# Optimization experiments

Hardware: AMD Instinct MI355X
Metric: run time of the kernel (lower is better)

The kernel has to match this reference:

```python
import jax, jax.numpy as jnp
import numpy as np

GAMMA = 0.99
ETA = 0.1
PHI = 0.9
EPS_FLOOR_NEWTON = 1e-8
EPS_FLOOR_BETA = 1e-6
N_NEWTON = 20


def _epsilon_cosh(r):
    # r: [B, N] nonnegative residuals; per-row Newton solve for epsilon s.t.
    # mean(sinh(r/eps)) == 1 along axis 1.
    N = r.shape[1]
    r_max = jnp.maximum(jnp.max(r, axis=1, keepdims=True), EPS_FLOOR_NEWTON)
    eps = r_max / (jnp.log(jnp.asarray(2.0 * N, dtype=r.dtype)) + EPS_FLOOR_NEWTON)
    for _ in range(N_NEWTON):
        eps_safe = jnp.maximum(eps, EPS_FLOOR_NEWTON)
        u = r / eps_safe  # [B, N]
        val = jnp.mean(jnp.sinh(u), axis=1, keepdims=True) - 1.0
        grad = jnp.mean(jnp.cosh(u) * (-u / eps_safe), axis=1, keepdims=True)
        eps = eps - val / (grad - EPS_FLOOR_NEWTON)
    return jnp.maximum(eps, EPS_FLOOR_NEWTON)


def _update_spatial_weights(r_i, Lambda, it):
    # 'cosh' weighting potential branch of update_spatial_weights
    del it  # unused by the cosh branch
    eps_q = _epsilon_cosh(r_i)                       # [B, 1]
    beta = 1.0 / (eps_q + EPS_FLOOR_BETA)            # [B, 1]
    q = jnp.sinh(beta * r_i)                         # [B, N]
    q_max = jnp.max(q, axis=1, keepdims=True)
    q_norm = q / (q_max + 1e-20)
    lambda_it = PHI * q_norm + (1.0 - PHI)
    return GAMMA * Lambda + ETA * lambda_it


def setup_inputs() -> dict:
    key = jax.random.key(0)
    k1, k2, k3 = jax.random.split(key, 3)
    B, N = 2048, 8192
    y_pred = jax.random.normal(k1, (B, N), dtype=jnp.float32)
    y_true = jax.random.normal(k2, (B, N), dtype=jnp.float32)
    Lambda = jax.random.uniform(k3, (B, N), dtype=jnp.float32)
    return {"y_pred": y_pred, "y_true": y_true, "Lambda": Lambda, "it": 100}


def reference(y_pred, y_true, Lambda, it):
    r_i = jnp.abs(y_true - y_pred)
    # weights are computed on detached residuals
    updated_Lambda = _update_spatial_weights(jax.lax.stop_gradient(r_i), Lambda, it)
    loss = jnp.mean(jnp.square(updated_Lambda * r_i))
    return (loss, updated_Lambda)
```

## Files before the change

### kernel.cpp

```cpp
#include <hip/hip_runtime.h>
#include <math.h>

#define N_COLS 8192
#define BLOCK  256
#define NW     4
#define F4PT   (N_COLS / BLOCK / 4)
#define NBINS  1024
#define BPL    (NBINS / 64)

__global__ void zero_out_kernel(float* out) {
    if (threadIdx.x == 0 && blockIdx.x == 0) out[0] = 0.0f;
}

__global__ __launch_bounds__(BLOCK) void custom_loss_kernel(
        const float* __restrict__ y_pred,
        const float* __restrict__ y_true,
        const float* __restrict__ Lambda,
        float* __restrict__ out,
        float inv_total) {
    __shared__ unsigned int s_hist[NBINS];
    __shared__ float s_wmax[NW];
    __shared__ float s_part[NW];
    __shared__ float s_bcast[2];

    const int row  = blockIdx.x;
    const int tid  = threadIdx.x;
    const int lane = tid & 63;
    const int wid  = tid >> 6;
    const size_t base = (size_t)row * N_COLS;
    const float4* yp4 = (const float4*)(y_pred + base);
    const float4* yt4 = (const float4*)(y_true + base);

    float4 r[F4PT];
    float rmax = 0.0f;
    #pragma unroll
    for (int j = 0; j < F4PT; ++j) {
        const int g = j * BLOCK + tid;
        float4 a = yt4[g];
        float4 b = yp4[g];
        float4 rv;
        rv.x = fabsf(a.x - b.x); rv.y = fabsf(a.y - b.y);
        rv.z = fabsf(a.z - b.z); rv.w = fabsf(a.w - b.w);
        r[j] = rv;
        rmax = fmaxf(rmax, fmaxf(fmaxf(rv.x, rv.y), fmaxf(rv.z, rv.w)));
    }
    #pragma unroll
    for (int m = 32; m >= 1; m >>= 1) rmax = fmaxf(rmax, __shfl_xor(rmax, m, 64));
    #pragma unroll
    for (int i = 0; i < NBINS / BLOCK; ++i) s_hist[tid + i * BLOCK] = 0u;
    __syncthreads();
    if (lane == 0) s_wmax[wid] = rmax;
    __syncthreads();
    rmax = fmaxf(fmaxf(s_wmax[0], s_wmax[1]), fmaxf(s_wmax[2], s_wmax[3]));
    rmax = fmaxf(rmax, 1e-8f);

    const float hscale = (float)NBINS / rmax;
    #pragma unroll
    for (int j = 0; j < F4PT; ++j) {
        unsigned bx = min((unsigned)(r[j].x * hscale), (unsigned)(NBINS - 1));
        unsigned by = min((unsigned)(r[j].y * hscale), (unsigned)(NBINS - 1));
        unsigned bz = min((unsigned)(r[j].z * hscale), (unsigned)(NBINS - 1));
        unsigned bw = min((unsigned)(r[j].w * hscale), (unsigned)(NBINS - 1));
        atomicAdd(&s_hist[bx], 1u);
        atomicAdd(&s_hist[by], 1u);
        atomicAdd(&s_hist[bz], 1u);
        atomicAdd(&s_hist[bw], 1u);
    }
    __syncthreads();

    if (wid == 0) {
        float eps = rmax / (logf(2.0f * (float)N_COLS) + 1e-8f);
        const float binw = rmax * (1.0f / (float)NBINS);
        const float sc2  = 0.5f / (float)N_COLS;
        for (int it = 0; it < 20; ++it) {
            const float inv_eps = 1.0f / fmaxf(eps, 1e-8f);
            float fs = 0.0f, gs = 0.0f;
            #pragma unroll
            for (int k = 0; k < BPL; ++k) {
                const int b = lane + 64 * k;
                float n = (float)s_hist[b];
                float m = ((float)b + 0.5f) * binw;
                float u = m * inv_eps;
                float e  = __expf(u);
                float ei = __expf(-u);
                fs = fmaf(n, e - ei, fs);
                gs = fmaf(n * (e + ei), u, gs);
            }
            #pragma unroll
            for (int m2 = 32; m2 >= 1; m2 >>= 1) {
                fs += __shfl_xor(fs, m2, 64);
                gs += __shfl_xor(gs, m2, 64);
            }
            float val  = fmaf(fs, sc2, -1.0f);
            float grad = -(gs * sc2) * inv_eps;
            float delta = val / (grad - 1e-8f);
            eps -= delta;
            if (fabsf(delta) <= 1e-5f * eps) break;
        }
        eps = fmaxf(eps, 1e-8f);
        const float beta = 1.0f / (eps + 1e-6f);
        const float um = beta * rmax;
        const float qmax = 0.5f * (__expf(um) - __expf(-um));
        if (lane == 0) {
            s_bcast[0] = beta;
            s_bcast[1] = 1.0f / (qmax + 1e-20f);
        }
    }
    __syncthreads();
    const float beta     = s_bcast[0];
    const float inv_qmax = s_bcast[1];

    const float4* lam4 = (const float4*)(Lambda + base);
    float* outw = out + 1 + base;
    float s_loss = 0.0f;
    #pragma unroll
    for (int j = 0; j < F4PT; ++j) {
        const int g = j * BLOCK + tid;
        float4 L = lam4[g];
        float rr[4] = {r[j].x, r[j].y, r[j].z, r[j].w};
        float LL[4] = {L.x, L.y, L.z, L.w};
        #pragma unroll
        for (int c = 0; c < 4; ++c) {
            float u  = beta * rr[c];
            float q  = 0.5f * (__expf(u) - __expf(-u));
            float lam_it = fmaf(0.9f, q * inv_qmax, 0.1f);
            float uL = fmaf(0.99f, LL[c], 0.1f * lam_it);
            outw[(size_t)g * 4 + c] = uL;
            float t = uL * rr[c];
            s_loss = fmaf(t, t, s_loss);
        }
    }
    #pragma unroll
    for (int m = 32; m >= 1; m >>= 1) s_loss += __shfl_xor(s_loss, m, 64);
    __syncthreads();
    if (lane == 0) s_part[wid] = s_loss;
    __syncthreads();
    if (tid == 0) {
        float tot = (s_part[0] + s_part[1]) + (s_part[2] + s_part[3]);
        atomicAdd(out, tot * inv_total);
    }
}

extern "C" void kernel_launch(void* const* d_in, const int* in_sizes, int n_in,
                              void* d_out, int out_size, void* d_ws, size_t ws_size,
                              hipStream_t stream) {
    const float* y_pred = (const float*)d_in[0];
    const float* y_true = (const float*)d_in[1];
    const float* Lambda = (const float*)d_in[2];
    float* out = (float*)d_out;

    const int total = in_sizes[0];
    const int B = total / N_COLS;
    const float inv_total = 1.0f / (float)total;

    hipLaunchKernelGGL(zero_out_kernel, dim3(1), dim3(64), 0, stream, out);
    hipLaunchKernelGGL(custom_loss_kernel, dim3(B), dim3(BLOCK), 0, stream,
                       y_pred, y_true, Lambda, out, inv_total);
}
```

Measured before the change: 226.0 us.

## Bin residuals by float exponent bits and run Newton solve redundantly per wave

Histogram bins now come straight from the float bit pattern (a log-spaced range with a fixed offset), so binning no longer waits for the block-wide max reduction and can overlap it. Every wave now runs the Newton iteration itself on register-cached bins, which removes the serial single-wave phase and the broadcast barrier. Lambda is prefetched together with the residual loads. The cost is more registers (Lambda held in registers, bins per lane) and a fixed bin range that may clip very small or very large residuals, which can change accuracy.

```diff
diff --git a/kernel.cpp b/kernel.cpp
--- a/kernel.cpp
+++ b/kernel.cpp
@@ -1,12 +1,13 @@
 #include <hip/hip_runtime.h>
 #include <math.h>
 
-#define N_COLS 8192
-#define BLOCK  256
-#define NW     4
-#define F4PT   (N_COLS / BLOCK / 4)
-#define NBINS  1024
-#define BPL    (NBINS / 64)
+#define N_COLS  8192
+#define BLOCK   256
+#define VPT     (N_COLS / BLOCK)
+#define F4PT    (VPT / 4)
+#define NBINS   1024
+#define BIN_OFF 7360
+#define BPL     (NBINS / 64)
 
 __global__ void zero_out_kernel(float* out) {
     if (threadIdx.x == 0 && blockIdx.x == 0) out[0] = 0.0f;
@@ -18,26 +19,31 @@
         const float* __restrict__ Lambda,
         float* __restrict__ out,
         float inv_total) {
-    __shared__ unsigned int s_hist[NBINS];
-    __shared__ float s_wmax[NW];
-    __shared__ float s_part[NW];
-    __shared__ float s_bcast[2];
+    __shared__ unsigned s_hist[NBINS];
+    __shared__ float s_wmax[4];
+    __shared__ float s_part[4];
 
     const int row  = blockIdx.x;
     const int tid  = threadIdx.x;
     const int lane = tid & 63;
     const int wid  = tid >> 6;
     const size_t base = (size_t)row * N_COLS;
-    const float4* yp4 = (const float4*)(y_pred + base);
-    const float4* yt4 = (const float4*)(y_true + base);
+    const float4* yp4  = (const float4*)(y_pred + base);
+    const float4* yt4  = (const float4*)(y_true + base);
+    const float4* lam4 = (const float4*)(Lambda + base);
+
+    #pragma unroll
+    for (int i = 0; i < NBINS / BLOCK; ++i) s_hist[tid + i * BLOCK] = 0u;
+    __syncthreads();
 
     float4 r[F4PT];
+    float4 L[F4PT];
     float rmax = 0.0f;
     #pragma unroll
     for (int j = 0; j < F4PT; ++j) {
         const int g = j * BLOCK + tid;
-        float4 a = yt4[g];
-        float4 b = yp4[g];
+        float4 a = yt4[g], b = yp4[g];
+        L[j] = lam4[g];
         float4 rv;
         rv.x = fabsf(a.x - b.x); rv.y = fabsf(a.y - b.y);
         rv.z = fabsf(a.z - b.z); rv.w = fabsf(a.w - b.w);
@@ -45,80 +51,65 @@
         rmax = fmaxf(rmax, fmaxf(fmaxf(rv.x, rv.y), fmaxf(rv.z, rv.w)));
     }
     #pragma unroll
+    for (int j = 0; j < F4PT; ++j) {
+        float rv[4] = {r[j].x, r[j].y, r[j].z, r[j].w};
+        #pragma unroll
+        for (int c = 0; c < 4; ++c) {
+            int idx = (int)(__float_as_uint(rv[c]) >> 17) - BIN_OFF;
+            idx = min(max(idx, 0), NBINS - 1);
+            atomicAdd(&s_hist[idx], 1u);
+        }
+    }
+    #pragma unroll
     for (int m = 32; m >= 1; m >>= 1) rmax = fmaxf(rmax, __shfl_xor(rmax, m, 64));
-    #pragma unroll
-    for (int i = 0; i < NBINS / BLOCK; ++i) s_hist[tid + i * BLOCK] = 0u;
-    __syncthreads();
     if (lane == 0) s_wmax[wid] = rmax;
     __syncthreads();
-    rmax = fmaxf(fmaxf(s_wmax[0], s_wmax[1]), fmaxf(s_wmax[2], s_wmax[3]));
-    rmax = fmaxf(rmax, 1e-8f);
+    rmax = fmaxf(fmaxf(fmaxf(s_wmax[0], s_wmax[1]),
+                       fmaxf(s_wmax[2], s_wmax[3])), 1e-8f);
 
-    const float hscale = (float)NBINS / rmax;
+    float n[BPL], m[BPL];
     #pragma unroll
-    for (int j = 0; j < F4PT; ++j) {
-        unsigned bx = min((unsigned)(r[j].x * hscale), (unsigned)(NBINS - 1));
-        unsigned by = min((unsigned)(r[j].y * hscale), (unsigned)(NBINS - 1));
-        unsigned bz = min((unsigned)(r[j].z * hscale), (unsigned)(NBINS - 1));
-        unsigned bw = min((unsigned)(r[j].w * hscale), (unsigned)(NBINS - 1));
-        atomicAdd(&s_hist[bx], 1u);
-        atomicAdd(&s_hist[by], 1u);
-        atomicAdd(&s_hist[bz], 1u);
-        atomicAdd(&s_hist[bw], 1u);
+    for (int i = 0; i < BPL; ++i) {
+        const int b = lane + 64 * i;
+        n[i] = (float)s_hist[b];
+        m[i] = __uint_as_float(((unsigned)(b + BIN_OFF) << 17) | 0x10000u);
     }
-    __syncthreads();
+    float eps = rmax / (logf(2.0f * (float)N_COLS) + 1e-8f);
+    const float sc2 = 0.5f / (float)N_COLS;
+    for (int it = 0; it < 20; ++it) {
+        const float inv_eps = 1.0f / fmaxf(eps, 1e-8f);
+        float fs = 0.0f, gs = 0.0f;
+        #pragma unroll
+        for (int i = 0; i < BPL; ++i) {
+            float u  = m[i] * inv_eps;
+            float e  = __expf(u);
+            float ei = __expf(-u);
+            fs = fmaf(n[i], e - ei, fs);
+            gs = fmaf(n[i] * (e + ei), u, gs);
+        }
+        #pragma unroll
+        for (int s = 32; s >= 1; s >>= 1) {
+            fs += __shfl_xor(fs, s, 64);
+            gs += __shfl_xor(gs, s, 64);
+        }
+        float val  = fmaf(fs, sc2, -1.0f);
+        float grad = -(gs * sc2) * inv_eps;
+        float delta = val / (grad - 1e-8f);
+        eps -= delta;
+        if (fabsf(delta) <= 1e-5f * eps) break;
+    }
+    eps = fmaxf(eps, 1e-8f);
+    const float beta = 1.0f / (eps + 1e-6f);
+    const float um = beta * rmax;
+    const float inv_qmax = 1.0f / (0.5f * (__expf(um) - __expf(-um)) + 1e-20f);
 
-    if (wid == 0) {
-        float eps = rmax / (logf(2.0f * (float)N_COLS) + 1e-8f);
-        const float binw = rmax * (1.0f / (float)NBINS);
-        const float sc2  = 0.5f / (float)N_COLS;
-        for (int it = 0; it < 20; ++it) {
-            const float inv_eps = 1.0f / fmaxf(eps, 1e-8f);
-            float fs = 0.0f, gs = 0.0f;
-            #pragma unroll
-            for (int k = 0; k < BPL; ++k) {
-                const int b = lane + 64 * k;
-                float n = (float)s_hist[b];
-                float m = ((float)b + 0.5f) * binw;
-                float u = m * inv_eps;
-                float e  = __expf(u);
-                float ei = __expf(-u);
-                fs = fmaf(n, e - ei, fs);
-                gs = fmaf(n * (e + ei), u, gs);
-            }
-            #pragma unroll
-            for (int m2 = 32; m2 >= 1; m2 >>= 1) {
-                fs += __shfl_xor(fs, m2, 64);
-                gs += __shfl_xor(gs, m2, 64);
-            }
-            float val  = fmaf(fs, sc2, -1.0f);
-            float grad = -(gs * sc2) * inv_eps;
-            float delta = val / (grad - 1e-8f);
-            eps -= delta;
-            if (fabsf(delta) <= 1e-5f * eps) break;
-        }
-        eps = fmaxf(eps, 1e-8f);
-        const float beta = 1.0f / (eps + 1e-6f);
-        const float um = beta * rmax;
-        const float qmax = 0.5f * (__expf(um) - __expf(-um));
-        if (lane == 0) {
-            s_bcast[0] = beta;
-            s_bcast[1] = 1.0f / (qmax + 1e-20f);
-        }
-    }
-    __syncthreads();
-    const float beta     = s_bcast[0];
-    const float inv_qmax = s_bcast[1];
-
-    const float4* lam4 = (const float4*)(Lambda + base);
     float* outw = out + 1 + base;
     float s_loss = 0.0f;
     #pragma unroll
     for (int j = 0; j < F4PT; ++j) {
         const int g = j * BLOCK + tid;
-        float4 L = lam4[g];
         float rr[4] = {r[j].x, r[j].y, r[j].z, r[j].w};
-        float LL[4] = {L.x, L.y, L.z, L.w};
+        float LL[4] = {L[j].x, L[j].y, L[j].z, L[j].w};
         #pragma unroll
         for (int c = 0; c < 4; ++c) {
             float u  = beta * rr[c];
@@ -131,7 +122,7 @@
         }
     }
     #pragma unroll
-    for (int m = 32; m >= 1; m >>= 1) s_loss += __shfl_xor(s_loss, m, 64);
+    for (int s = 32; s >= 1; s >>= 1) s_loss += __shfl_xor(s_loss, s, 64);
     __syncthreads();
     if (lane == 0) s_part[wid] = s_loss;
     __syncthreads();
```

New measurement: 229.0 us. About the same (+1.3%).
